# Optimization experiments

Hardware: AMD Instinct MI355X
Metric: run time of the kernel (lower is better)

Reference implementation:

```python
import jax, jax.numpy as jnp
import numpy as np

B, S, D, E, K = 4, 2048, 1024, 8, 2
H = 4 * D  # SwiGLU hidden size


def setup_inputs() -> dict:
    key = jax.random.key(0)
    ks = jax.random.split(key, 6)
    s = 0.02
    return {
        "x": jax.random.normal(ks[0], (B, S, D), dtype=jnp.float32),
        "Wr": jax.random.normal(ks[1], (D, E), dtype=jnp.float32) * s,
        "br": jnp.zeros((E,), jnp.float32),
        "Wg": jax.random.normal(ks[2], (E, D, H), dtype=jnp.float32) * s,
        "bg": jnp.zeros((E, H), jnp.float32),
        "Wu": jax.random.normal(ks[3], (E, D, H), dtype=jnp.float32) * s,
        "bu": jnp.zeros((E, H), jnp.float32),
        "Wd": jax.random.normal(ks[4], (E, H, D), dtype=jnp.float32) * s,
        "bd": jnp.zeros((E, D), jnp.float32),
        "top_k": K,
    }


def reference(x, Wr, br, Wg, bg, Wu, bu, Wd, bd, top_k):
    # Router: top-k over expert logits, softmax over the selected k values.
    Bx, Sx, Dx = x.shape
    Ex = Wr.shape[-1]
    logits = x @ Wr + br                              # [B,S,E]
    vals, idx = jax.lax.top_k(logits, top_k)          # [B,S,K]
    probs = jax.nn.softmax(vals, axis=-1)             # [B,S,K]
    # Dense per-token expert weight; 0 for experts the token is not routed to.
    gate_w = jnp.sum(jax.nn.one_hot(idx, Ex, dtype=x.dtype) * probs[..., None], axis=-2)  # [B,S,E]

    xt = x.reshape(-1, Dx)          # [T,D]
    gw = gate_w.reshape(-1, Ex).T   # [E,T]

    def body(acc, p):
        wg, bgi, wu, bui, wd, bdi, ge = p
        h = jax.nn.silu(xt @ wg + bgi) * (xt @ wu + bui)   # [T,4D]
        y = (h @ wd + bdi) * ge[:, None]                   # zero where ge==0 (not routed)
        return acc + y, None

    out, _ = jax.lax.scan(body, jnp.zeros_like(xt), (Wg, bg, Wu, bu, Wd, bd, gw))
    return out.reshape(Bx, Sx, Dx)
```

## Files before the change

kernel.cpp:

```cpp
#include <hip/hip_runtime.h>
#include <hip/hip_fp16.h>


#define T_TOK 8192
#define D_IN  1024
#define E_EXP 8
#define H_HID 4096
#define NSLOT (T_TOK * 2)
#define NSLOT_PAD (NSLOT + 256)
#define KSPLIT 4

typedef _Float16 f16;
typedef __attribute__((ext_vector_type(8))) _Float16 f16x8;
typedef __attribute__((ext_vector_type(4))) _Float16 f16x4;
typedef __attribute__((ext_vector_type(4))) float f32x4;

__device__ __forceinline__ void gload_lds16(const void* g, void* l) {
  __builtin_amdgcn_global_load_lds(
      (const __attribute__((address_space(1))) unsigned int*)g,
      (__attribute__((address_space(3))) unsigned int*)l, 16, 0, 0);
}


__global__ __launch_bounds__(256) void prep_kernel(
    const float* __restrict__ x, const float* __restrict__ Wr,
    const float* __restrict__ br, const float* __restrict__ Wg,
    const float* __restrict__ Wu, const float* __restrict__ Wd,
    int* __restrict__ eidx, float2* __restrict__ pval,
    int* __restrict__ counts, f16* __restrict__ xb,
    f16* __restrict__ wgut, f16* __restrict__ wdt) {
  __shared__ float tile[128][33];
  int g = blockIdx.x;
  if (g < T_TOK / 4) {
    int lane = threadIdx.x & 63, wid = threadIdx.x >> 6;
    int t = g * 4 + wid;
    const float* xr = x + (size_t)t * D_IN;
    float s[8] = {0.f, 0.f, 0.f, 0.f, 0.f, 0.f, 0.f, 0.f};
    int dbase = lane * 16;
#pragma unroll
    for (int i = 0; i < 4; ++i) {
      float4 xv = *(const float4*)(xr + dbase + i * 4);
      f16x4 xo = {(f16)xv.x, (f16)xv.y, (f16)xv.z, (f16)xv.w};
      *(f16x4*)(xb + (size_t)t * D_IN + dbase + i * 4) = xo;
      const float xs[4] = {xv.x, xv.y, xv.z, xv.w};
#pragma unroll
      for (int j = 0; j < 4; ++j) {
        const float* wr = Wr + (size_t)(dbase + i * 4 + j) * E_EXP;
        float4 w0 = *(const float4*)wr;
        float4 w1 = *(const float4*)(wr + 4);
        float xvj = xs[j];
        s[0] += xvj * w0.x; s[1] += xvj * w0.y; s[2] += xvj * w0.z; s[3] += xvj * w0.w;
        s[4] += xvj * w1.x; s[5] += xvj * w1.y; s[6] += xvj * w1.z; s[7] += xvj * w1.w;
      }
    }
#pragma unroll
    for (int off = 32; off; off >>= 1)
#pragma unroll
      for (int e = 0; e < 8; ++e) s[e] += __shfl_xor(s[e], off);
    if (lane == 0) {
      float v[8];
#pragma unroll
      for (int e = 0; e < 8; ++e) v[e] = s[e] + br[e];
      int i0 = 0; float v0 = v[0];
#pragma unroll
      for (int e = 1; e < 8; ++e) if (v[e] > v0) { v0 = v[e]; i0 = e; }
      int i1 = -1; float v1 = -1e30f;
#pragma unroll
      for (int e = 0; e < 8; ++e)
        if (e != i0 && v[e] > v1) { v1 = v[e]; i1 = e; }
      float ed = __expf(v1 - v0);
      float inv = 1.f / (1.f + ed);
      eidx[t] = i0 | (i1 << 8);
      pval[t] = make_float2(inv, ed * inv);
      atomicAdd(&counts[i0], 1);
      atomicAdd(&counts[i1], 1);
    }
    return;
  }
  int i = g - T_TOK / 4;
  int which = i >> 13;
  int j = i & 8191;
  const float* src; f16* dst; int R, C, MAP, cx, cy, e; size_t dstride;
  if (which < 2) {
    cx = j & 127; cy = (j >> 7) & 7; e = j >> 10;
    R = D_IN; C = H_HID; dstride = (size_t)2 * H_HID * D_IN;
    dst = wgut; src = (which == 0) ? Wg : Wu; MAP = which + 1;
  } else {
    cx = j & 31; cy = (j >> 5) & 31; e = j >> 10;
    R = H_HID; C = D_IN; dstride = (size_t)D_IN * H_HID;
    dst = wdt; src = Wd; MAP = 0;
  }
  const float* s = src + (size_t)e * R * C;
  f16* d = dst + (size_t)e * dstride;
  int c0 = cx * 32, r0 = cy * 128;
#pragma unroll
  for (int q4 = 0; q4 < 4; ++q4) {
    int q = q4 * 256 + threadIdx.x;
    int r = q >> 3, c4 = (q & 7) * 4;
    float4 v = *(const float4*)(s + (size_t)(r0 + r) * C + c0 + c4);
    tile[r][c4 + 0] = v.x; tile[r][c4 + 1] = v.y;
    tile[r][c4 + 2] = v.z; tile[r][c4 + 3] = v.w;
  }
  __syncthreads();
#pragma unroll
  for (int w2 = 0; w2 < 2; ++w2) {
    int w = w2 * 256 + threadIdx.x;
    int col = w >> 4, oct = w & 15;
    int c = c0 + col;
    int ro = (MAP == 0) ? c : (((c >> 4) << 5) + ((MAP == 2) ? 16 : 0) + (c & 15));
    f16x8 o;
#pragma unroll
    for (int k = 0; k < 8; ++k) o[k] = (f16)tile[oct * 8 + k][col];
    *(f16x8*)(d + (size_t)ro * R + r0 + oct * 8) = o;
  }
}

__global__ void scan_kernel(const int* __restrict__ counts, int* __restrict__ offsets) {
  if (threadIdx.x == 0) {
    int acc = 0;
#pragma unroll
    for (int e = 0; e < E_EXP; ++e) { offsets[e] = acc; acc += counts[e]; }
    offsets[E_EXP] = acc;
  }
}

__global__ __launch_bounds__(256) void scatter_kernel(
    const int* __restrict__ eidx, const float2* __restrict__ pval,
    const int* __restrict__ offsets, int* __restrict__ cursors,
    int* __restrict__ perm, float* __restrict__ gatew, int2* __restrict__ slotAB) {
  int t = blockIdx.x * 256 + threadIdx.x;
  if (t >= T_TOK) return;
  int ei = eidx[t];
  float2 p = pval[t];
  int e0 = ei & 0xff, e1 = (ei >> 8) & 0xff;
  int s0 = offsets[e0] + atomicAdd(&cursors[e0], 1);
  perm[s0] = t; gatew[s0] = p.x;
  int s1 = offsets[e1] + atomicAdd(&cursors[e1], 1);
  perm[s1] = t; gatew[s1] = p.y;
  slotAB[t] = make_int2(s0, s1);
}


#define BAR __builtin_amdgcn_s_barrier()
#define VMCNT(N) asm volatile("s_waitcnt vmcnt(" #N ")" ::: "memory")

#define STAGE_(B, ISB, H, KT, BASE) do {                                   \
  char* d_ = smem + (B)*65536 + (ISB)*32768 + (H)*16384 + wid*1024;        \
  gload_lds16(BASE[(H)*2+0] + (size_t)(KT)*64, d_);                        \
  gload_lds16(BASE[(H)*2+1] + (size_t)(KT)*64, d_ + 8192);                 \
} while (0)

#define LDA_(B, Q)                                                          \
  _Pragma("unroll")                                                         \
  for (int m_ = 0; m_ < 4; ++m_) {                                          \
    fa[m_][0] = *(const f16x8*)(smem + (B)*65536 + aoff + ((Q)*4+m_)*2048 + offk0); \
    fa[m_][1] = *(const f16x8*)(smem + (B)*65536 + aoff + ((Q)*4+m_)*2048 + offk1); \
  }

#define LDB_(FB, B, RH)                                                     \
  _Pragma("unroll")                                                         \
  for (int n_ = 0; n_ < 2; ++n_) {                                          \
    FB[n_][0] = *(const f16x8*)(smem + (B)*65536 + 32768 + boff + ((RH)*2+n_)*2048 + offk0); \
    FB[n_][1] = *(const f16x8*)(smem + (B)*65536 + 32768 + boff + ((RH)*2+n_)*2048 + offk1); \
  }

#define QUAD_(Q, RH, FB)                                                    \
  __builtin_amdgcn_s_setprio(1);                                            \
  _Pragma("unroll")                                                         \
  for (int m_ = 0; m_ < 4; ++m_)                                            \
    _Pragma("unroll")                                                       \
    for (int n_ = 0; n_ < 2; ++n_) {                                        \
      acc[(Q)*4+m_][(RH)*2+n_] = __builtin_amdgcn_mfma_f32_16x16x32_f16(    \
          fa[m_][0], FB[n_][0], acc[(Q)*4+m_][(RH)*2+n_], 0, 0, 0);         \
      acc[(Q)*4+m_][(RH)*2+n_] = __builtin_amdgcn_mfma_f32_16x16x32_f16(    \
          fa[m_][1], FB[n_][1], acc[(Q)*4+m_][(RH)*2+n_], 0, 0, 0);         \
    }                                                                       \
  __builtin_amdgcn_s_setprio(0);

template<int MODE>
__global__ __launch_bounds__(512, 2) void ffn_8ph_kernel(
    const f16* __restrict__ Asrc, const f16* __restrict__ Bsrc,
    const float* __restrict__ bias0, const float* __restrict__ bias1,
    const int* __restrict__ offsets, const int* __restrict__ perm,
    const float* __restrict__ gatew, f16* __restrict__ dst) {
  constexpr int KD = MODE ? H_HID : D_IN;
  constexpr int BROWS = MODE ? D_IN : 2 * H_HID;
  constexpr int NT = 16;

  __shared__ __align__(16) char smem[131072];

  int g = blockIdx.x;
  int xcd = g & 7;
  int mt = (g >> 3) & 31;
  int e, nt, kc;
  if constexpr (MODE == 0) {
    int panel = xcd + 8 * (g >> 8);
    e = panel >> 5; nt = panel & 31; kc = 0;
  } else {
    int sp = xcd + 8 * (g >> 8);
    e = sp >> 4; nt = (sp >> 2) & 3; kc = sp & 3;
  }

  int off = offsets[e];
  int cnt = offsets[e + 1] - off;
  if (mt * 256 >= cnt) return;

  int tid = threadIdx.x, lane = tid & 63, wid = tid >> 6;
  int wm = wid >> 2, wn = wid & 3;
  int l15 = lane & 15, lc0 = lane >> 4, s7 = l15 & 7;
  int aoff = (wm * 128 + l15) * 128;
  int boff = (wn * 64 + l15) * 128;
  int offk0 = ((lc0) ^ s7) * 16;
  int offk1 = ((lc0 + 4) ^ s7) * 16;

  int rowh_[2], lc_[2];
#pragma unroll
  for (int i = 0; i < 2; ++i) {
    int chunk = (i * 8 + wid) * 64 + lane;
    rowh_[i] = chunk >> 3;
    lc_[i] = (chunk & 7) ^ (rowh_[i] & 7);
  }

  const f16 *aB[4], *bB[4];
#pragma unroll
  for (int h = 0; h < 2; ++h)
#pragma unroll
    for (int i = 0; i < 2; ++i) {
      int absrow = h * 128 + rowh_[i];
      bB[h * 2 + i] = Bsrc + ((size_t)e * BROWS + nt * 256 + absrow) * KD +
                      kc * 1024 + lc_[i] * 8;
      int slot = off + min(mt * 256 + absrow, cnt - 1);
      if constexpr (MODE == 0)
        aB[h * 2 + i] = Asrc + (size_t)perm[slot] * KD + lc_[i] * 8;
      else
        aB[h * 2 + i] = Asrc + (size_t)slot * KD + kc * 1024 + lc_[i] * 8;
    }

  float bv0[4], bv1[2];
  if constexpr (MODE == 0) {
#pragma unroll
    for (int p = 0; p < 2; ++p) {
      int h = nt * 128 + wn * 32 + p * 16 + l15;
      bv0[p] = bias0[e * H_HID + h];
      bv1[p] = bias1[e * H_HID + h];
    }
  } else {
#pragma unroll
    for (int n = 0; n < 4; ++n)
      bv0[n] = (kc == 0)
                   ? bias0[e * D_IN + nt * 256 + wn * 64 + n * 16 + l15]
                   : 0.f;
  }

  f32x4 acc[8][4] = {};
  f16x8 fa[4][2], fb01[2][2], fb23[2][2];

  STAGE_(0, 1, 0, 0, bB); STAGE_(0, 1, 1, 0, bB);
  STAGE_(0, 0, 0, 0, aB); STAGE_(0, 0, 1, 0, aB);
  STAGE_(1, 1, 0, 1, bB); STAGE_(1, 1, 1, 1, bB);
  STAGE_(1, 0, 0, 1, aB);
  VMCNT(6);
  BAR;

  for (int it = 0; it < NT / 2; ++it) {
    int b_ = 2 * it + 1;
    int a2 = min(2 * it + 2, NT - 1);
    int b2 = min(2 * it + 3, NT - 1);
    LDA_(0, 0); LDB_(fb01, 0, 0); STAGE_(1, 0, 1, b_, aB);
    BAR; QUAD_(0, 0, fb01); BAR;
    LDB_(fb23, 0, 1);
    BAR; QUAD_(0, 1, fb23); BAR;
    LDA_(0, 1); STAGE_(0, 1, 0, a2, bB);
    BAR; QUAD_(1, 0, fb01); BAR;
    STAGE_(0, 1, 1, a2, bB);
    BAR; QUAD_(1, 1, fb23);
    VMCNT(4);
    BAR;
    LDA_(1, 0); LDB_(fb01, 1, 0); STAGE_(0, 0, 0, a2, aB);
    BAR; QUAD_(0, 0, fb01); BAR;
    LDB_(fb23, 1, 1); STAGE_(0, 0, 1, a2, aB);
    BAR; QUAD_(0, 1, fb23); BAR;
    LDA_(1, 1); STAGE_(1, 1, 0, b2, bB);
    BAR; QUAD_(1, 0, fb01); BAR;
    STAGE_(1, 1, 1, b2, bB); STAGE_(1, 0, 0, b2, aB);
    BAR; QUAD_(1, 1, fb23);
    VMCNT(6);
    BAR;
  }

  VMCNT(0);
  __syncthreads();

  int c0_ = lc0 * 4;
  f16* tile = (f16*)smem;
  if constexpr (MODE == 0) {
#pragma unroll
    for (int p = 0; p < 2; ++p) {
      int colL = wn * 32 + p * 16 + l15;
#pragma unroll
      for (int m = 0; m < 8; ++m) {
        int row = wm * 128 + m * 16 + c0_;
#pragma unroll
        for (int r = 0; r < 4; ++r) {
          float gv = acc[m][2 * p][r] + bv0[p];
          float uv = acc[m][2 * p + 1][r] + bv1[p];
          tile[(row + r) * 128 + colL] = (f16)((gv / (1.f + __expf(-gv))) * uv);
        }
      }
    }
    __syncthreads();
    f16* dbase = dst + (size_t)(off + mt * 256) * H_HID + nt * 128;
#pragma unroll
    for (int i = 0; i < 8; ++i) {
      int linear = i * 512 + tid;
      int row = linear >> 4, c16 = linear & 15;
      if (mt * 256 + row < cnt) {
        f16x8 v = *(const f16x8*)&tile[row * 128 + c16 * 8];
        __builtin_nontemporal_store(v, (f16x8*)(dbase + (size_t)row * H_HID + c16 * 8));
      }
    }
  } else {
#pragma unroll
    for (int n = 0; n < 4; ++n) {
      int colL = wn * 64 + n * 16 + l15;
#pragma unroll
      for (int m = 0; m < 8; ++m) {
        int row = wm * 128 + m * 16 + c0_;
#pragma unroll
        for (int r = 0; r < 4; ++r) {
          int slot = off + min(mt * 256 + row + r, cnt - 1);
          tile[(row + r) * 256 + colL] =
              (f16)(gatew[slot] * (acc[m][n][r] + bv0[n]));
        }
      }
    }
    __syncthreads();
    f16* dstP = dst + (size_t)kc * NSLOT_PAD * D_IN;
    f16* dbase = dstP + (size_t)(off + mt * 256) * D_IN + nt * 256;
#pragma unroll
    for (int i = 0; i < 16; ++i) {
      int linear = i * 512 + tid;
      int row = linear >> 5, c16 = linear & 31;
      if (mt * 256 + row < cnt) {
        f16x8 v = *(const f16x8*)&tile[row * 256 + c16 * 8];
        __builtin_nontemporal_store(v, (f16x8*)(dbase + (size_t)row * D_IN + c16 * 8));
      }
    }
  }
}

__global__ __launch_bounds__(256) void combine_kernel(
    const f16* __restrict__ ypart, const int2* __restrict__ slotAB,
    float* __restrict__ out) {
  int i = blockIdx.x * 256 + threadIdx.x;
  int t = i >> 7;
  int c8 = i & 127;
  int2 s = slotAB[t];
  float sum[8] = {0.f, 0.f, 0.f, 0.f, 0.f, 0.f, 0.f, 0.f};
#pragma unroll
  for (int kc = 0; kc < KSPLIT; ++kc) {
    const f16* base = ypart + (size_t)kc * NSLOT_PAD * D_IN + c8 * 8;
    f16x8 y0 = *(const f16x8*)(base + (size_t)s.x * D_IN);
    f16x8 y1 = *(const f16x8*)(base + (size_t)s.y * D_IN);
#pragma unroll
    for (int j = 0; j < 8; ++j) sum[j] += (float)y0[j] + (float)y1[j];
  }
  float* o = out + (size_t)t * D_IN + c8 * 8;
  f32x4 o0 = {sum[0], sum[1], sum[2], sum[3]};
  f32x4 o1 = {sum[4], sum[5], sum[6], sum[7]};
  __builtin_nontemporal_store(o0, (f32x4*)o);
  __builtin_nontemporal_store(o1, (f32x4*)(o + 4));
}


extern "C" void kernel_launch(void* const* d_in, const int* in_sizes, int n_in,
                              void* d_out, int out_size, void* d_ws, size_t ws_size,
                              hipStream_t stream) {
  const float* x  = (const float*)d_in[0];
  const float* Wr = (const float*)d_in[1];
  const float* br = (const float*)d_in[2];
  const float* Wg = (const float*)d_in[3];
  const float* bg = (const float*)d_in[4];
  const float* Wu = (const float*)d_in[5];
  const float* bu = (const float*)d_in[6];
  const float* Wd = (const float*)d_in[7];
  const float* bd = (const float*)d_in[8];
  float* out = (float*)d_out;

  char* ws = (char*)d_ws;
  size_t o = 0;
  auto alloc = [&](size_t bytes) {
    size_t r = o;
    o += (bytes + 255) & ~(size_t)255;
    return r;
  };
  f16* xb     = (f16*)(ws + alloc((size_t)T_TOK * D_IN * 2));
  f16* wgut   = (f16*)(ws + alloc((size_t)E_EXP * 2 * H_HID * D_IN * 2));
  f16* wdt    = (f16*)(ws + alloc((size_t)E_EXP * D_IN * H_HID * 2));
  f16* hbuf   = (f16*)(ws + alloc((size_t)NSLOT_PAD * H_HID * 2));
  int* eidx   = (int*)(ws + alloc((size_t)T_TOK * 4));
  float2* pval= (float2*)(ws + alloc((size_t)T_TOK * 8));
  int* counts = (int*)(ws + alloc(64 * 4));
  int* cursors = counts + 8;
  int* offsets = counts + 16;
  int* perm   = (int*)(ws + alloc((size_t)NSLOT_PAD * 4));
  float* gatew= (float*)(ws + alloc((size_t)NSLOT_PAD * 4));
  int2* slotAB= (int2*)(ws + alloc((size_t)T_TOK * 8));
  f16* ypart  = xb;

  hipMemsetAsync(counts, 0, 64 * 4, stream);

  prep_kernel<<<dim3(T_TOK / 4 + 3 * 8192), 256, 0, stream>>>(
      x, Wr, br, Wg, Wu, Wd, eidx, pval, counts, xb, wgut, wdt);
  scan_kernel<<<1, 64, 0, stream>>>(counts, offsets);
  scatter_kernel<<<T_TOK / 256, 256, 0, stream>>>(eidx, pval, offsets, cursors,
                                                  perm, gatew, slotAB);
  ffn_8ph_kernel<0><<<dim3(8192), 512, 0, stream>>>(
      xb, wgut, bg, bu, offsets, perm, nullptr, hbuf);
  ffn_8ph_kernel<1><<<dim3(4096), 512, 0, stream>>>(
      hbuf, wdt, bd, nullptr, offsets, nullptr, gatew, ypart);
  combine_kernel<<<T_TOK * D_IN / 8 / 256, 256, 0, stream>>>(ypart, slotAB, out);
}
```

Measured before the change: 912.3 us.

## Store hidden activations and down-proj weights in K-split chunk-major layout

The intermediate hidden buffer and the transposed down-projection weights are reorganized into four contiguous 1024-wide K chunks, so each split-K down-projection block reads a dense row stride of 1024 rather than strided 4096-wide rows. The gate/up kernel writes its output tile into the matching chunk, and the prep kernel writes Wd into the chunked layout. The aim is better DRAM page and cache locality for the down-projection loads, at the cost of more complex indexing.

```diff
diff --git a/kernel.cpp b/kernel.cpp
--- a/kernel.cpp
+++ b/kernel.cpp
@@ -80,18 +80,16 @@
   int i = g - T_TOK / 4;
   int which = i >> 13;
   int j = i & 8191;
-  const float* src; f16* dst; int R, C, MAP, cx, cy, e; size_t dstride;
+  const float* src; int C, cx, cy, e;
   if (which < 2) {
     cx = j & 127; cy = (j >> 7) & 7; e = j >> 10;
-    R = D_IN; C = H_HID; dstride = (size_t)2 * H_HID * D_IN;
-    dst = wgut; src = (which == 0) ? Wg : Wu; MAP = which + 1;
+    C = H_HID; src = (which == 0) ? Wg : Wu;
   } else {
     cx = j & 31; cy = (j >> 5) & 31; e = j >> 10;
-    R = H_HID; C = D_IN; dstride = (size_t)D_IN * H_HID;
-    dst = wdt; src = Wd; MAP = 0;
-  }
+    C = D_IN; src = Wd;
+  }
+  int R = (which < 2) ? D_IN : H_HID;
   const float* s = src + (size_t)e * R * C;
-  f16* d = dst + (size_t)e * dstride;
   int c0 = cx * 32, r0 = cy * 128;
 #pragma unroll
   for (int q4 = 0; q4 < 4; ++q4) {
@@ -107,11 +105,16 @@
     int w = w2 * 256 + threadIdx.x;
     int col = w >> 4, oct = w & 15;
     int c = c0 + col;
-    int ro = (MAP == 0) ? c : (((c >> 4) << 5) + ((MAP == 2) ? 16 : 0) + (c & 15));
     f16x8 o;
 #pragma unroll
     for (int k = 0; k < 8; ++k) o[k] = (f16)tile[oct * 8 + k][col];
-    *(f16x8*)(d + (size_t)ro * R + r0 + oct * 8) = o;
+    if (which < 2) {
+      int ro = ((c >> 4) << 5) + ((which == 1) ? 16 : 0) + (c & 15);
+      *(f16x8*)(wgut + ((size_t)e * 2 * H_HID + ro) * D_IN + r0 + oct * 8) = o;
+    } else {
+      int kc = cy >> 3, k0 = (cy & 7) * 128;
+      *(f16x8*)(wdt + (((size_t)e * 4 + kc) * 1024 + c) * 1024 + k0 + oct * 8) = o;
+    }
   }
 }
 
@@ -183,8 +186,6 @@
     const float* __restrict__ bias0, const float* __restrict__ bias1,
     const int* __restrict__ offsets, const int* __restrict__ perm,
     const float* __restrict__ gatew, f16* __restrict__ dst) {
-  constexpr int KD = MODE ? H_HID : D_IN;
-  constexpr int BROWS = MODE ? D_IN : 2 * H_HID;
   constexpr int NT = 16;
 
   __shared__ __align__(16) char smem[131072];
@@ -227,13 +228,16 @@
 #pragma unroll
     for (int i = 0; i < 2; ++i) {
       int absrow = h * 128 + rowh_[i];
-      bB[h * 2 + i] = Bsrc + ((size_t)e * BROWS + nt * 256 + absrow) * KD +
-                      kc * 1024 + lc_[i] * 8;
       int slot = off + min(mt * 256 + absrow, cnt - 1);
-      if constexpr (MODE == 0)
-        aB[h * 2 + i] = Asrc + (size_t)perm[slot] * KD + lc_[i] * 8;
-      else
-        aB[h * 2 + i] = Asrc + (size_t)slot * KD + kc * 1024 + lc_[i] * 8;
+      if constexpr (MODE == 0) {
+        bB[h * 2 + i] = Bsrc + ((size_t)e * 2 * H_HID + nt * 256 + absrow) * 1024 +
+                        lc_[i] * 8;
+        aB[h * 2 + i] = Asrc + (size_t)perm[slot] * 1024 + lc_[i] * 8;
+      } else {
+        bB[h * 2 + i] = Bsrc + (((size_t)e * 4 + kc) * 1024 + nt * 256 + absrow) * 1024 +
+                        lc_[i] * 8;
+        aB[h * 2 + i] = Asrc + ((size_t)kc * NSLOT_PAD + slot) * 1024 + lc_[i] * 8;
+      }
     }
 
   float bv0[4], bv1[2];
@@ -309,14 +313,15 @@
       }
     }
     __syncthreads();
-    f16* dbase = dst + (size_t)(off + mt * 256) * H_HID + nt * 128;
+    f16* dbase = dst + ((size_t)(nt >> 3) * NSLOT_PAD + off + mt * 256) * 1024 +
+                 (nt & 7) * 128;
 #pragma unroll
     for (int i = 0; i < 8; ++i) {
       int linear = i * 512 + tid;
       int row = linear >> 4, c16 = linear & 15;
       if (mt * 256 + row < cnt) {
         f16x8 v = *(const f16x8*)&tile[row * 128 + c16 * 8];
-        __builtin_nontemporal_store(v, (f16x8*)(dbase + (size_t)row * H_HID + c16 * 8));
+        __builtin_nontemporal_store(v, (f16x8*)(dbase + (size_t)row * 1024 + c16 * 8));
       }
     }
   } else {
@@ -397,7 +402,7 @@
   f16* xb     = (f16*)(ws + alloc((size_t)T_TOK * D_IN * 2));
   f16* wgut   = (f16*)(ws + alloc((size_t)E_EXP * 2 * H_HID * D_IN * 2));
   f16* wdt    = (f16*)(ws + alloc((size_t)E_EXP * D_IN * H_HID * 2));
-  f16* hbuf   = (f16*)(ws + alloc((size_t)NSLOT_PAD * H_HID * 2));
+  f16* hbuf   = (f16*)(ws + alloc((size_t)KSPLIT * NSLOT_PAD * 1024 * 2));
   int* eidx   = (int*)(ws + alloc((size_t)T_TOK * 4));
   float2* pval= (float2*)(ws + alloc((size_t)T_TOK * 8));
   int* counts = (int*)(ws + alloc(64 * 4));
```

Result: no change. 926.5 us (+1.5%).
